# Kernel optimization log

Hardware: AMD Instinct MI355X
Metric: run time of the kernel (lower is better)

Reference implementation:

```python
import jax, jax.numpy as jnp
import numpy as np

DIM = 1024
CODEBOOK_SIZE = 8192
CODEBOOK_DIM = 16
NUM_CODEBOOKS = 4
BATCH = 4
SEQ = 1024
LN_EPS = 1e-5
COS_EPS = 1e-8  # torch cosine_similarity eps


def setup_inputs() -> dict:
    key = jax.random.key(0)
    k1, k2, k3 = jax.random.split(key, 3)
    x = jax.random.normal(k1, (BATCH, SEQ, DIM), dtype=jnp.float32)
    # xavier_normal_: std = sqrt(2 / (fan_in + fan_out)) over last two dims
    xavier_std = float(np.sqrt(2.0 / (DIM + CODEBOOK_DIM)))
    rand_projs = jax.random.normal(k2, (NUM_CODEBOOKS, DIM, CODEBOOK_DIM), dtype=jnp.float32) * xavier_std
    cb = jax.random.normal(k3, (NUM_CODEBOOKS, CODEBOOK_SIZE, CODEBOOK_DIM), dtype=jnp.float32)
    cb = cb / jnp.clip(jnp.linalg.norm(cb, axis=-1, keepdims=True), 1e-12, None)  # F.normalize
    return {"x": x, "rand_projs": rand_projs, "CB": cb}


def reference(x, rand_projs, CB):
    # LayerNorm(dim, elementwise_affine=False)
    mean = jnp.mean(x, axis=-1, keepdims=True)
    var = jnp.mean(jnp.square(x - mean), axis=-1, keepdims=True)
    xn = (x - mean) * jax.lax.rsqrt(var + LN_EPS)
    # random projection: (b,t,d),(h,d,k) -> (h,b,t,k)
    proj = jnp.einsum('btd,hdk->hbtk', xn, rand_projs)
    # cosine similarity == normalize both then dot (torch clamps norm at eps)
    proj_n = proj / jnp.maximum(jnp.linalg.norm(proj, axis=-1, keepdims=True), COS_EPS)
    cb_n = CB / jnp.maximum(jnp.linalg.norm(CB, axis=-1, keepdims=True), COS_EPS)
    # distances: (h,b,t,cs)  (matches torch stack(h,b,cs,t).permute(0,1,3,2))
    distances = jnp.einsum('hbtk,hck->hbtc', proj_n, cb_n)
    # indices: argmax over codebook, stacked (h,b,t) -> permute(1,2,0) -> (b,t,h)
    indices = jnp.argmax(distances, axis=-1).transpose(1, 2, 0)
    return indices, distances
```

## Files before the change

kernel.cpp:

```cpp
#include <hip/hip_runtime.h>
#include <hip/hip_bf16.h>

#define NH 4
#define BT 4096
#define DD 1024
#define CK 16
#define CS 8192

typedef float vfloat4 __attribute__((ext_vector_type(4)));

#define WS_STATS 0
#define WS_PART  8192
#define WS_PROJN 1056768
#define WS_CBN   1318912

__global__ __launch_bounds__(256) void k_stats(const float* __restrict__ x,
                                               float* __restrict__ stats) {
  const int lane = threadIdx.x & 63;
  const int row  = blockIdx.x * 4 + (threadIdx.x >> 6);
  const float4* xr = reinterpret_cast<const float4*>(x + (size_t)row * DD);
  float4 v[4];
  float s = 0.f;
#pragma unroll
  for (int i = 0; i < 4; ++i) {
    v[i] = xr[lane + 64 * i];
    s += (v[i].x + v[i].y) + (v[i].z + v[i].w);
  }
#pragma unroll
  for (int m = 32; m >= 1; m >>= 1) s += __shfl_xor(s, m, 64);
  const float mean = s * (1.f / DD);
  float vs = 0.f;
#pragma unroll
  for (int i = 0; i < 4; ++i) {
    float a = v[i].x - mean, b = v[i].y - mean, c = v[i].z - mean, d = v[i].w - mean;
    vs += (a * a + b * b) + (c * c + d * d);
  }
#pragma unroll
  for (int m = 32; m >= 1; m >>= 1) vs += __shfl_xor(vs, m, 64);
  if (lane == 0) {
    stats[2 * row]     = mean;
    stats[2 * row + 1] = rsqrtf(vs * (1.f / DD) + 1e-5f);
  }
}

__global__ __launch_bounds__(256) void k_proj(const float* __restrict__ x,
                                              const float* __restrict__ stats,
                                              const float* __restrict__ P,
                                              float* __restrict__ part) {
  __shared__ float xa[32][68];
  __shared__ float pa[32][68];
  const int tile = blockIdx.x & 63;
  const int ds   = blockIdx.x >> 6;
  const int tid  = threadIdx.x;
  const int tx = tid & 15, ty = tid >> 4;
  const int r0 = ty * 4, o0 = tx * 4;
  float acc[4][4] = {};

  for (int dc = 0; dc < 256; dc += 32) {
    const int d0 = ds * 256 + dc;
    {
      const int row  = tid >> 2;
      const int rowg = tile * 64 + row;
      const float mean = stats[2 * rowg];
      const float rstd = stats[2 * rowg + 1];
      const float* xp = x + (size_t)rowg * DD + d0 + (tid & 3) * 8;
      float4 a = reinterpret_cast<const float4*>(xp)[0];
      float4 b = reinterpret_cast<const float4*>(xp)[1];
      const int dd = (tid & 3) * 8;
      xa[dd + 0][row] = (a.x - mean) * rstd;
      xa[dd + 1][row] = (a.y - mean) * rstd;
      xa[dd + 2][row] = (a.z - mean) * rstd;
      xa[dd + 3][row] = (a.w - mean) * rstd;
      xa[dd + 4][row] = (b.x - mean) * rstd;
      xa[dd + 5][row] = (b.y - mean) * rstd;
      xa[dd + 6][row] = (b.z - mean) * rstd;
      xa[dd + 7][row] = (b.w - mean) * rstd;
    }
    {
      const int h  = tid >> 6;
      const int f0 = (tid & 63) * 8;
      const float* pp = P + (size_t)h * DD * CK + (size_t)d0 * CK + f0;
      float4 a = reinterpret_cast<const float4*>(pp)[0];
      float4 b = reinterpret_cast<const float4*>(pp)[1];
      float vv[8] = {a.x, a.y, a.z, a.w, b.x, b.y, b.z, b.w};
#pragma unroll
      for (int j = 0; j < 8; ++j) {
        int f = f0 + j;
        pa[f >> 4][(h << 4) | (f & 15)] = vv[j];
      }
    }
    __syncthreads();
#pragma unroll
    for (int d = 0; d < 32; ++d) {
      float4 xv = *reinterpret_cast<const float4*>(&xa[d][r0]);
      float4 pv = *reinterpret_cast<const float4*>(&pa[d][o0]);
      float xr[4] = {xv.x, xv.y, xv.z, xv.w};
      float pr[4] = {pv.x, pv.y, pv.z, pv.w};
#pragma unroll
      for (int i = 0; i < 4; ++i)
#pragma unroll
        for (int j = 0; j < 4; ++j) acc[i][j] = fmaf(xr[i], pr[j], acc[i][j]);
    }
    __syncthreads();
  }
  float* pb = part + ((size_t)ds * BT + tile * 64) * 64;
#pragma unroll
  for (int i = 0; i < 4; ++i) {
    float4 o = {acc[i][0], acc[i][1], acc[i][2], acc[i][3]};
    *reinterpret_cast<float4*>(pb + (size_t)(r0 + i) * 64 + o0) = o;
  }
}

__global__ __launch_bounds__(256) void k_norm(const float* __restrict__ part,
                                              float* __restrict__ proj_n) {
  const int t   = blockIdx.x * 256 + threadIdx.x;
  const int row = t >> 2, h = t & 3;
  float s[16];
#pragma unroll
  for (int k = 0; k < 16; ++k) s[k] = 0.f;
#pragma unroll
  for (int ds = 0; ds < 4; ++ds) {
    const float* pb = part + (size_t)ds * BT * 64 + (size_t)row * 64 + h * 16;
#pragma unroll
    for (int w = 0; w < 4; ++w) {
      float4 v = reinterpret_cast<const float4*>(pb)[w];
      s[w * 4 + 0] += v.x; s[w * 4 + 1] += v.y; s[w * 4 + 2] += v.z; s[w * 4 + 3] += v.w;
    }
  }
  float nsq = 0.f;
#pragma unroll
  for (int k = 0; k < 16; ++k) nsq = fmaf(s[k], s[k], nsq);
  const float inv = 1.f / fmaxf(sqrtf(nsq), 1e-8f);
  float* op = proj_n + ((size_t)h * BT + row) * 16;
#pragma unroll
  for (int w = 0; w < 4; ++w) {
    float4 v = {s[w*4+0] * inv, s[w*4+1] * inv, s[w*4+2] * inv, s[w*4+3] * inv};
    reinterpret_cast<float4*>(op)[w] = v;
  }
}

__global__ __launch_bounds__(256) void k_cbn(const float* __restrict__ CB,
                                             float* __restrict__ cb_n) {
  const int t = blockIdx.x * 256 + threadIdx.x;
  const float4* src = reinterpret_cast<const float4*>(CB + (size_t)t * 16);
  float4 v[4];
  float nsq = 0.f;
#pragma unroll
  for (int w = 0; w < 4; ++w) {
    v[w] = src[w];
    nsq = fmaf(v[w].x, v[w].x, nsq); nsq = fmaf(v[w].y, v[w].y, nsq);
    nsq = fmaf(v[w].z, v[w].z, nsq); nsq = fmaf(v[w].w, v[w].w, nsq);
  }
  const float inv = 1.f / fmaxf(sqrtf(nsq), 1e-8f);
  float4* dst = reinterpret_cast<float4*>(cb_n + (size_t)t * 16);
#pragma unroll
  for (int w = 0; w < 4; ++w) {
    float4 o = {v[w].x * inv, v[w].y * inv, v[w].z * inv, v[w].w * inv};
    dst[w] = o;
  }
}

#define QLOAD(Q0, Q1, Q2, Q3, r)                              \
  Q0 = *reinterpret_cast<const float4*>(&q[(r)][0]);          \
  Q1 = *reinterpret_cast<const float4*>(&q[(r)][4]);          \
  Q2 = *reinterpret_cast<const float4*>(&q[(r)][8]);          \
  Q3 = *reinterpret_cast<const float4*>(&q[(r)][12]);

#define ROWBODY(r, Q0, Q1, Q2, Q3)                                         \
  {                                                                        \
    float dj[4];                                                           \
    _Pragma("unroll")                                                      \
    for (int j = 0; j < 4; ++j) {                                          \
      float s =        cb[j][0].x * Q0.x;                                  \
      s = fmaf(cb[j][0].y, Q0.y, s);                                       \
      s = fmaf(cb[j][0].z, Q0.z, s);                                       \
      s = fmaf(cb[j][0].w, Q0.w, s);                                       \
      s = fmaf(cb[j][1].x, Q1.x, s);                                       \
      s = fmaf(cb[j][1].y, Q1.y, s);                                       \
      s = fmaf(cb[j][1].z, Q1.z, s);                                       \
      s = fmaf(cb[j][1].w, Q1.w, s);                                       \
      s = fmaf(cb[j][2].x, Q2.x, s);                                       \
      s = fmaf(cb[j][2].y, Q2.y, s);                                       \
      s = fmaf(cb[j][2].z, Q2.z, s);                                       \
      s = fmaf(cb[j][2].w, Q2.w, s);                                       \
      s = fmaf(cb[j][3].x, Q3.x, s);                                       \
      s = fmaf(cb[j][3].y, Q3.y, s);                                       \
      s = fmaf(cb[j][3].z, Q3.z, s);                                       \
      s = fmaf(cb[j][3].w, Q3.w, s);                                       \
      dj[j] = s;                                                           \
    }                                                                      \
    vfloat4 dots = {dj[0], dj[1], dj[2], dj[3]};                           \
    __builtin_nontemporal_store(dots,                                      \
        reinterpret_cast<vfloat4*>(db + (size_t)(r) * CS + c));            \
    _Pragma("unroll")                                                      \
    for (int j = 0; j < 4; ++j) {                                          \
      if (dj[j] > best[(r)]) { best[(r)] = dj[j]; bidx[(r)] = c + j; }     \
    }                                                                      \
  }                                                                        \
  __builtin_amdgcn_sched_barrier(0);

__global__ __launch_bounds__(256, 3) void k_dist(const float* __restrict__ proj_n,
                                                 const float* __restrict__ cb_n,
                                                 float* __restrict__ dist,
                                                 float* __restrict__ idx_out) {
  __shared__ float q[8][16];
  __shared__ float redv[8][4];
  __shared__ int   redi[8][4];
  const int h    = blockIdx.x >> 9;
  const int tile = blockIdx.x & 511;
  const int tid  = threadIdx.x;

  if (tid < 32) {
    const int r = tid >> 2, k4 = tid & 3;
    float4 v = *reinterpret_cast<const float4*>(
        proj_n + ((size_t)h * BT + tile * 8 + r) * 16 + k4 * 4);
    *reinterpret_cast<float4*>(&q[r][k4 * 4]) = v;
  }
  __syncthreads();

  float best[8];
  int   bidx[8];
#pragma unroll
  for (int r = 0; r < 8; ++r) { best[r] = -2e30f; bidx[r] = 0; }

  const float* cbh = cb_n + (size_t)h * CS * CK;
  float* db = dist + ((size_t)h * BT + tile * 8) * CS;

  for (int cc = 0; cc < 8; ++cc) {
    const int c = cc * 1024 + tid * 4;
    float4 cb[4][4];
    const float4* cs = reinterpret_cast<const float4*>(cbh + (size_t)c * CK);
#pragma unroll
    for (int j = 0; j < 4; ++j)
#pragma unroll
      for (int w = 0; w < 4; ++w) cb[j][w] = cs[j * 4 + w];

    float4 qa0, qa1, qa2, qa3, qb0, qb1, qb2, qb3;
    QLOAD(qa0, qa1, qa2, qa3, 0)
    QLOAD(qb0, qb1, qb2, qb3, 1) ROWBODY(0, qa0, qa1, qa2, qa3)
    QLOAD(qa0, qa1, qa2, qa3, 2) ROWBODY(1, qb0, qb1, qb2, qb3)
    QLOAD(qb0, qb1, qb2, qb3, 3) ROWBODY(2, qa0, qa1, qa2, qa3)
    QLOAD(qa0, qa1, qa2, qa3, 4) ROWBODY(3, qb0, qb1, qb2, qb3)
    QLOAD(qb0, qb1, qb2, qb3, 5) ROWBODY(4, qa0, qa1, qa2, qa3)
    QLOAD(qa0, qa1, qa2, qa3, 6) ROWBODY(5, qb0, qb1, qb2, qb3)
    QLOAD(qb0, qb1, qb2, qb3, 7) ROWBODY(6, qa0, qa1, qa2, qa3)
    ROWBODY(7, qb0, qb1, qb2, qb3)
  }

  const int lane = tid & 63, wv = tid >> 6;
#pragma unroll
  for (int r = 0; r < 8; ++r) {
    float v = best[r];
    int   ii = bidx[r];
#pragma unroll
    for (int m = 32; m >= 1; m >>= 1) {
      float ov = __shfl_xor(v, m, 64);
      int   oi = __shfl_xor(ii, m, 64);
      if (ov > v || (ov == v && oi < ii)) { v = ov; ii = oi; }
    }
    if (lane == 0) { redv[r][wv] = v; redi[r][wv] = ii; }
  }
  __syncthreads();
  if (tid < 8) {
    const int r = tid;
    float v = redv[r][0];
    int   ii = redi[r][0];
#pragma unroll
    for (int w = 1; w < 4; ++w) {
      float ov = redv[r][w];
      int   oi = redi[r][w];
      if (ov > v || (ov == v && oi < ii)) { v = ov; ii = oi; }
    }
    const int rowg = tile * 8 + r;
    idx_out[(size_t)rowg * 4 + h] = (float)ii;
  }
}

extern "C" void kernel_launch(void* const* d_in, const int* in_sizes, int n_in,
                              void* d_out, int out_size, void* d_ws, size_t ws_size,
                              hipStream_t stream) {
  (void)in_sizes; (void)n_in; (void)out_size; (void)ws_size;
  const float* x  = (const float*)d_in[0];
  const float* P  = (const float*)d_in[1];
  const float* CB = (const float*)d_in[2];
  float* ws  = (float*)d_ws;
  float* out = (float*)d_out;
  float* idx_out = out;
  float* dist    = out + BT * NH;

  k_stats<<<1024, 256, 0, stream>>>(x, ws + WS_STATS);
  k_proj <<<256,  256, 0, stream>>>(x, ws + WS_STATS, P, ws + WS_PART);
  k_norm <<<64,   256, 0, stream>>>(ws + WS_PART, ws + WS_PROJN);
  k_cbn  <<<128,  256, 0, stream>>>(CB, ws + WS_CBN);
  k_dist <<<2048, 256, 0, stream>>>(ws + WS_PROJN, ws + WS_CBN, dist, idx_out);
}
```

Measured before the change: 172.8 us.

## Process 16 query rows per block and load queries directly from global

Doubles the number of query rows handled per block in the distance kernel, halving the grid size and the number of times each codebook chunk is loaded per row. Query vectors are now read straight from global memory (uniform addresses) instead of being staged through shared memory with a barrier. This raises per-thread register use for best/index tracking and reduces block count, which may hurt occupancy or wave balance.

```diff
diff --git a/kernel.cpp b/kernel.cpp
--- a/kernel.cpp
+++ b/kernel.cpp
@@ -160,11 +160,11 @@
   }
 }
 
-#define QLOAD(Q0, Q1, Q2, Q3, r)                              \
-  Q0 = *reinterpret_cast<const float4*>(&q[(r)][0]);          \
-  Q1 = *reinterpret_cast<const float4*>(&q[(r)][4]);          \
-  Q2 = *reinterpret_cast<const float4*>(&q[(r)][8]);          \
-  Q3 = *reinterpret_cast<const float4*>(&q[(r)][12]);
+#define QLOADG(Q0, Q1, Q2, Q3, r)  \
+  Q0 = qg[4 * (r) + 0];            \
+  Q1 = qg[4 * (r) + 1];            \
+  Q2 = qg[4 * (r) + 2];            \
+  Q3 = qg[4 * (r) + 3];
 
 #define ROWBODY(r, Q0, Q1, Q2, Q3)                                         \
   {                                                                        \
@@ -203,28 +203,21 @@
                                                  const float* __restrict__ cb_n,
                                                  float* __restrict__ dist,
                                                  float* __restrict__ idx_out) {
-  __shared__ float q[8][16];
-  __shared__ float redv[8][4];
-  __shared__ int   redi[8][4];
-  const int h    = blockIdx.x >> 9;
-  const int tile = blockIdx.x & 511;
+  __shared__ float redv[16][4];
+  __shared__ int   redi[16][4];
+  const int h    = blockIdx.x >> 8;
+  const int tile = blockIdx.x & 255;
   const int tid  = threadIdx.x;
 
-  if (tid < 32) {
-    const int r = tid >> 2, k4 = tid & 3;
-    float4 v = *reinterpret_cast<const float4*>(
-        proj_n + ((size_t)h * BT + tile * 8 + r) * 16 + k4 * 4);
-    *reinterpret_cast<float4*>(&q[r][k4 * 4]) = v;
-  }
-  __syncthreads();
-
-  float best[8];
-  int   bidx[8];
-#pragma unroll
-  for (int r = 0; r < 8; ++r) { best[r] = -2e30f; bidx[r] = 0; }
+  float best[16];
+  int   bidx[16];
+#pragma unroll
+  for (int r = 0; r < 16; ++r) { best[r] = -2e30f; bidx[r] = 0; }
 
   const float* cbh = cb_n + (size_t)h * CS * CK;
-  float* db = dist + ((size_t)h * BT + tile * 8) * CS;
+  const float4* qg = reinterpret_cast<const float4*>(
+      proj_n + ((size_t)h * BT + tile * 16) * 16);
+  float* db = dist + ((size_t)h * BT + tile * 16) * CS;
 
   for (int cc = 0; cc < 8; ++cc) {
     const int c = cc * 1024 + tid * 4;
@@ -236,20 +229,28 @@
       for (int w = 0; w < 4; ++w) cb[j][w] = cs[j * 4 + w];
 
     float4 qa0, qa1, qa2, qa3, qb0, qb1, qb2, qb3;
-    QLOAD(qa0, qa1, qa2, qa3, 0)
-    QLOAD(qb0, qb1, qb2, qb3, 1) ROWBODY(0, qa0, qa1, qa2, qa3)
-    QLOAD(qa0, qa1, qa2, qa3, 2) ROWBODY(1, qb0, qb1, qb2, qb3)
-    QLOAD(qb0, qb1, qb2, qb3, 3) ROWBODY(2, qa0, qa1, qa2, qa3)
-    QLOAD(qa0, qa1, qa2, qa3, 4) ROWBODY(3, qb0, qb1, qb2, qb3)
-    QLOAD(qb0, qb1, qb2, qb3, 5) ROWBODY(4, qa0, qa1, qa2, qa3)
-    QLOAD(qa0, qa1, qa2, qa3, 6) ROWBODY(5, qb0, qb1, qb2, qb3)
-    QLOAD(qb0, qb1, qb2, qb3, 7) ROWBODY(6, qa0, qa1, qa2, qa3)
-    ROWBODY(7, qb0, qb1, qb2, qb3)
+    QLOADG(qa0, qa1, qa2, qa3, 0)
+    QLOADG(qb0, qb1, qb2, qb3, 1)  ROWBODY(0,  qa0, qa1, qa2, qa3)
+    QLOADG(qa0, qa1, qa2, qa3, 2)  ROWBODY(1,  qb0, qb1, qb2, qb3)
+    QLOADG(qb0, qb1, qb2, qb3, 3)  ROWBODY(2,  qa0, qa1, qa2, qa3)
+    QLOADG(qa0, qa1, qa2, qa3, 4)  ROWBODY(3,  qb0, qb1, qb2, qb3)
+    QLOADG(qb0, qb1, qb2, qb3, 5)  ROWBODY(4,  qa0, qa1, qa2, qa3)
+    QLOADG(qa0, qa1, qa2, qa3, 6)  ROWBODY(5,  qb0, qb1, qb2, qb3)
+    QLOADG(qb0, qb1, qb2, qb3, 7)  ROWBODY(6,  qa0, qa1, qa2, qa3)
+    QLOADG(qa0, qa1, qa2, qa3, 8)  ROWBODY(7,  qb0, qb1, qb2, qb3)
+    QLOADG(qb0, qb1, qb2, qb3, 9)  ROWBODY(8,  qa0, qa1, qa2, qa3)
+    QLOADG(qa0, qa1, qa2, qa3, 10) ROWBODY(9,  qb0, qb1, qb2, qb3)
+    QLOADG(qb0, qb1, qb2, qb3, 11) ROWBODY(10, qa0, qa1, qa2, qa3)
+    QLOADG(qa0, qa1, qa2, qa3, 12) ROWBODY(11, qb0, qb1, qb2, qb3)
+    QLOADG(qb0, qb1, qb2, qb3, 13) ROWBODY(12, qa0, qa1, qa2, qa3)
+    QLOADG(qa0, qa1, qa2, qa3, 14) ROWBODY(13, qb0, qb1, qb2, qb3)
+    QLOADG(qb0, qb1, qb2, qb3, 15) ROWBODY(14, qa0, qa1, qa2, qa3)
+    ROWBODY(15, qb0, qb1, qb2, qb3)
   }
 
   const int lane = tid & 63, wv = tid >> 6;
 #pragma unroll
-  for (int r = 0; r < 8; ++r) {
+  for (int r = 0; r < 16; ++r) {
     float v = best[r];
     int   ii = bidx[r];
 #pragma unroll
@@ -261,7 +262,7 @@
     if (lane == 0) { redv[r][wv] = v; redi[r][wv] = ii; }
   }
   __syncthreads();
-  if (tid < 8) {
+  if (tid < 16) {
     const int r = tid;
     float v = redv[r][0];
     int   ii = redi[r][0];
@@ -271,7 +272,7 @@
       int   oi = redi[r][w];
       if (ov > v || (ov == v && oi < ii)) { v = ov; ii = oi; }
     }
-    const int rowg = tile * 8 + r;
+    const int rowg = tile * 16 + r;
     idx_out[(size_t)rowg * 4 + h] = (float)ii;
   }
 }
@@ -292,5 +293,5 @@
   k_proj <<<256,  256, 0, stream>>>(x, ws + WS_STATS, P, ws + WS_PART);
   k_norm <<<64,   256, 0, stream>>>(ws + WS_PART, ws + WS_PROJN);
   k_cbn  <<<128,  256, 0, stream>>>(CB, ws + WS_CBN);
-  k_dist <<<2048, 256, 0, stream>>>(ws + WS_PROJN, ws + WS_CBN, dist, idx_out);
-}
+  k_dist <<<1024, 256, 0, stream>>>(ws + WS_PROJN, ws + WS_CBN, dist, idx_out);
+}
```

After: 144.9 us, median of 2. 1.19x faster.
